# Kernel optimization log

Measured on AMD Instinct MI355X. Metric: run time of the kernel, lower is better.

## Reference

```python
import jax, jax.numpy as jnp
import numpy as np

ALPHA = 4.0          # spikingjelly default surrogate.Sigmoid(alpha=4.0)
V_TH = 1.0           # IFNode default v_threshold
BN_EPS = 1e-5

@jax.custom_vjp
def spike(x):
    # heaviside forward
    return (x >= 0.0).astype(x.dtype)

def _spike_fwd(x):
    return spike(x), x

def _spike_bwd(x, g):
    s = jax.nn.sigmoid(ALPHA * x)
    return (g * ALPHA * s * (1.0 - s),)

spike.defvjp(_spike_fwd, _spike_bwd)

def if_node(x_seq):
    """Multi-step IF neuron: integrate, threshold, hard reset (v_reset=0),
    detach_reset=True. x_seq: [T, ...] -> spikes [T, ...]."""
    def step(v, xt):
        v = v + xt
        s = spike(v - V_TH)
        v = v * (1.0 - jax.lax.stop_gradient(s))  # detached hard reset to 0
        return v, s
    _, s_seq = jax.lax.scan(step, jnp.zeros_like(x_seq[0]), x_seq)
    return s_seq

def bn1d(x, gamma, beta):
    """Training-mode BatchNorm1d over flattened (T*B) batch dim. x: [T,B,F]."""
    m = x.mean(axis=(0, 1))
    v = x.var(axis=(0, 1))  # biased variance, matches torch normalization
    return (x - m) * jax.lax.rsqrt(v + BN_EPS) * gamma + beta

def setup_inputs() -> dict:
    key = jax.random.key(0)
    ks = jax.random.split(key, 12)
    T, B, C, H, W = 8, 64, 2, 128, 128
    F0, D, NC = C * H * W, 2048, 1000
    x = jax.random.uniform(ks[0], (T, B, C, H, W), dtype=jnp.float32)
    def kaiming(k, out_f, in_f):
        # kaiming_normal_ mode='fan_out', relu gain: std = sqrt(2/out_f)
        return jax.random.normal(k, (out_f, in_f), dtype=jnp.float32) * np.sqrt(2.0 / out_f)
    def bias(k, out_f, in_f):
        bound = 1.0 / np.sqrt(in_f)
        return jax.random.uniform(k, (out_f,), dtype=jnp.float32, minval=-bound, maxval=bound)
    inp = {"x": x}
    dims = [(D, F0), (D, D), (D, D)]
    for i, (o, f) in enumerate(dims):
        inp[f"W{i}"] = kaiming(ks[1 + i], o, f)
        inp[f"b{i}"] = bias(ks[4 + i], o, f)
        inp[f"g{i}"] = jnp.ones((o,), jnp.float32)
        inp[f"be{i}"] = jnp.zeros((o,), jnp.float32)
    inp["Wout"] = kaiming(ks[7], NC, D)
    inp["bout"] = bias(ks[8], NC, D)
    return inp

def reference(x, W0, b0, g0, be0, W1, b1, g1, be1, W2, b2, g2, be2, Wout, bout):
    T, B = x.shape[0], x.shape[1]
    h = x.reshape(T, B, -1)           # [T,B,32768]
    h = if_node(h)                    # sn0
    for Wl, bl, gl, bel in ((W0, b0, g0, be0), (W1, b1, g1, be1), (W2, b2, g2, be2)):
        h = jnp.einsum('tbi,oi->tbo', h, Wl) + bl
        h = bn1d(h, gl, bel)
        h = if_node(h)
    out = jnp.einsum('tbi,oi->tbo', h, Wout) + bout  # [T,B,1000]
    return out.mean(axis=0)           # [B,1000]
```

## Files before the change

kernel.cpp:

```cpp
#include <hip/hip_runtime.h>


#define T_STEPS 8
#define BATCH 64
#define F0 32768
#define DIM 2048
#define NROWS 512
#define NC 1000

typedef __attribute__((ext_vector_type(8))) short short8;
typedef __attribute__((ext_vector_type(4))) float f32x4;

__device__ __forceinline__ unsigned short bf16_rne(float f) {
    unsigned int u = __float_as_uint(f);
    u += 0x7FFFu + ((u >> 16) & 1u);
    return (unsigned short)(u >> 16);
}

#define BM 128
#define BN 128
#define BK 64

#define SBAR() do { __builtin_amdgcn_sched_barrier(0); \
                    __builtin_amdgcn_s_barrier();      \
                    __builtin_amdgcn_sched_barrier(0); } while (0)

__device__ __forceinline__ short8 lds_frag(const unsigned short* base, int row, int kb) {
    const int off = row * 128 + (kb ^ ((row & 7) << 4));
    return *(const short8*)((const char*)base + off);
}

__global__ __launch_bounds__(512) void gemm_splitk(
    const unsigned short* __restrict__ A, const float* __restrict__ W,
    float* __restrict__ part, int M, int N, int K, int Kpart, int Wrows)
{
    __shared__ unsigned short As[2][BM * BK];
    __shared__ unsigned short Hs[BN * BK];
    __shared__ unsigned short Ls[BN * BK];

    const int gx = gridDim.x, gy = gridDim.y;
    const int nwg = gx * gy * gridDim.z;
    const int lid = blockIdx.x + gx * (blockIdx.y + gy * blockIdx.z);
    const int cpx = nwg >> 3;
    const int nid = (lid & 7) * cpx + (lid >> 3);
    const int bx  = nid % gx;
    const int by  = (nid / gx) % gy;
    const int kz  = nid / (gx * gy);

    const int tid  = threadIdx.x;
    const int lane = tid & 63;
    const int w    = tid >> 6;
    const int bm   = bx * BM;
    const int bn   = by * BN;
    const int ksteps = Kpart / BK;
    const int wm = (w >> 2) * 64;
    const int wn = (w & 3) * 32;
    const int kbase = kz * Kpart;

    f32x4 acc[4][2] = {};
    float4 wv[4];

    auto issue_loads = [&](int buf, int kt) {
        const int k0 = kbase + kt * BK;
#pragma unroll
        for (int i = 0; i < 4; ++i) {
            const int n  = (tid >> 4) + 32 * i;
            const int c4 = tid & 15;
            const int gn = min(bn + n, Wrows - 1);
            wv[i] = *(const float4*)&W[(size_t)gn * K + k0 + c4 * 4];
        }
#pragma unroll
        for (int c = 0; c < 2; ++c) {
            const int r    = w * 16 + c * 8 + (lane >> 3);
            const int colb = ((lane & 7) * 16) ^ ((r & 7) << 4);
            const char* src = (const char*)A + ((size_t)(bm + r) * K + k0) * 2 + colb;
            unsigned short* dst = &As[buf][(w * 16 + c * 8) * BK];
            __builtin_amdgcn_global_load_lds(
                (const __attribute__((address_space(1))) void*)src,
                (__attribute__((address_space(3))) void*)dst, 16, 0, 0);
        }
    };

    auto convert_write = [&]() {
#pragma unroll
        for (int i = 0; i < 4; ++i) {
            const int n  = (tid >> 4) + 32 * i;
            const int c4 = tid & 15;
            const float vf[4] = {wv[i].x, wv[i].y, wv[i].z, wv[i].w};
            unsigned short h[4], l[4];
#pragma unroll
            for (int e = 0; e < 4; ++e) {
                h[e] = bf16_rne(vf[e]);
                const float hf = __uint_as_float((unsigned int)h[e] << 16);
                l[e] = bf16_rne(vf[e] - hf);
            }
            const int off = n * 128 + ((c4 * 8) ^ ((n & 7) << 4));
            *(ushort4*)((char*)Hs + off) = make_ushort4(h[0], h[1], h[2], h[3]);
            *(ushort4*)((char*)Ls + off) = make_ushort4(l[0], l[1], l[2], l[3]);
        }
    };

    issue_loads(0, 0);
    convert_write();
    asm volatile("s_waitcnt vmcnt(0) lgkmcnt(0)" ::: "memory");
    SBAR();

    int cur = 0;
    for (int kt = 0; kt < ksteps; ++kt) {
        const bool last = (kt + 1 == ksteps);
        if (!last) issue_loads(cur ^ 1, kt + 1);

#pragma unroll
        for (int kk = 0; kk < 2; ++kk) {
            const int kb = (kk * 32 + (lane >> 4) * 8) * 2;
            short8 a[4], bh[2], bl[2];
#pragma unroll
            for (int i = 0; i < 4; ++i)
                a[i] = lds_frag(&As[cur][0], wm + i * 16 + (lane & 15), kb);
#pragma unroll
            for (int i = 0; i < 2; ++i) {
                const int r = wn + i * 16 + (lane & 15);
                bh[i] = lds_frag(Hs, r, kb);
                bl[i] = lds_frag(Ls, r, kb);
            }
#pragma unroll
            for (int mi = 0; mi < 4; ++mi)
#pragma unroll
                for (int ni = 0; ni < 2; ++ni) {
                    acc[mi][ni] = __builtin_amdgcn_mfma_f32_16x16x32_bf16(
                        a[mi], bh[ni], acc[mi][ni], 0, 0, 0);
                    acc[mi][ni] = __builtin_amdgcn_mfma_f32_16x16x32_bf16(
                        a[mi], bl[ni], acc[mi][ni], 0, 0, 0);
                }
        }

        if (!last) {
            SBAR();
            convert_write();
            asm volatile("s_waitcnt vmcnt(0) lgkmcnt(0)" ::: "memory");
            SBAR();
            cur ^= 1;
        }
    }

    const size_t zoff = (size_t)kz * M * N;
#pragma unroll
    for (int mi = 0; mi < 4; ++mi) {
        const int gr0 = bm + wm + mi * 16 + (lane >> 4) * 4;
#pragma unroll
        for (int ni = 0; ni < 2; ++ni) {
            const int gc = bn + wn + ni * 16 + (lane & 15);
            if (gc < N) {
#pragma unroll
                for (int e = 0; e < 4; ++e) {
                    const int gr = gr0 + e;
                    if (gr < M) part[zoff + (size_t)gr * N + gc] = acc[mi][ni][e];
                }
            }
        }
    }
}

__global__ __launch_bounds__(256) void reduce_bias(
    const float* __restrict__ part, const float* __restrict__ bias,
    float* __restrict__ out, int KS, int MN, int N)
{
    const int i4 = blockIdx.x * 256 + threadIdx.x;
    if (i4 * 4 >= MN) return;
    float4 s = make_float4(0.f, 0.f, 0.f, 0.f);
    for (int z = 0; z < KS; ++z) {
        const float4 p = *(const float4*)&part[(size_t)z * MN + i4 * 4];
        s.x += p.x; s.y += p.y; s.z += p.z; s.w += p.w;
    }
    const int col = (i4 * 4) % N;
    const float4 b = *(const float4*)&bias[col];
    s.x += b.x; s.y += b.y; s.z += b.z; s.w += b.w;
    *(float4*)&out[(size_t)i4 * 4] = s;
}

__global__ __launch_bounds__(256) void if0_kernel(
    const float* __restrict__ x, unsigned short* __restrict__ s)
{
    const size_t id4 = ((size_t)blockIdx.x * 256 + threadIdx.x) * 4;
    float v0 = 0.f, v1 = 0.f, v2 = 0.f, v3 = 0.f;
#pragma unroll
    for (int t = 0; t < T_STEPS; ++t) {
        const size_t idx = (size_t)t * (BATCH * (size_t)F0) + id4;
        const float4 xv = *(const float4*)&x[idx];
        ushort4 o;
        v0 += xv.x; if (v0 >= 1.f) { o.x = 0x3F80; v0 = 0.f; } else o.x = 0;
        v1 += xv.y; if (v1 >= 1.f) { o.y = 0x3F80; v1 = 0.f; } else o.y = 0;
        v2 += xv.z; if (v2 >= 1.f) { o.z = 0x3F80; v2 = 0.f; } else o.z = 0;
        v3 += xv.w; if (v3 >= 1.f) { o.w = 0x3F80; v3 = 0.f; } else o.w = 0;
        *(ushort4*)&s[idx] = o;
    }
}

__global__ __launch_bounds__(256) void bn_stats_if(
    const float* __restrict__ z, const float* __restrict__ g,
    const float* __restrict__ be, unsigned short* __restrict__ s)
{
    __shared__ float ssum[4][64], ssq[4][64];
    __shared__ float ssc[64], ssh[64];
    const int l = threadIdx.x & 63;
    const int q = threadIdx.x >> 6;
    const int f = blockIdx.x * 64 + l;
    float sum = 0.f, sq = 0.f;
    for (int r = q; r < NROWS; r += 4) {
        const float v = z[(size_t)r * DIM + f];
        sum += v; sq += v * v;
    }
    ssum[q][l] = sum; ssq[q][l] = sq;
    __syncthreads();
    if (threadIdx.x < 64) {
        float ts = 0.f, tq = 0.f;
#pragma unroll
        for (int i = 0; i < 4; ++i) { ts += ssum[i][l]; tq += ssq[i][l]; }
        const float mean = ts * (1.0f / NROWS);
        const float var  = tq * (1.0f / NROWS) - mean * mean;
        const float inv  = rsqrtf(var + 1e-5f);
        const float sc   = g[f] * inv;
        ssc[l] = sc;
        ssh[l] = be[f] - mean * sc;
    }
    __syncthreads();
    const float sc = ssc[l];
    const float sh = ssh[l];
    for (int b = q; b < BATCH; b += 4) {
        const int id = b * DIM + f;
        float v = 0.f;
#pragma unroll
        for (int t = 0; t < T_STEPS; ++t) {
            const size_t idx = (size_t)t * (BATCH * DIM) + id;
            v += z[idx] * sc + sh;
            if (v >= 1.0f) { s[idx] = 0x3F80; v = 0.f; }
            else           { s[idx] = 0; }
        }
    }
}

__global__ __launch_bounds__(256) void bn_stats_if_mean(
    const float* __restrict__ z, const float* __restrict__ g,
    const float* __restrict__ be, unsigned short* __restrict__ sbar)
{
    __shared__ float ssum[4][64], ssq[4][64];
    __shared__ float ssc[64], ssh[64];
    const int l = threadIdx.x & 63;
    const int q = threadIdx.x >> 6;
    const int f = blockIdx.x * 64 + l;
    float sum = 0.f, sq = 0.f;
    for (int r = q; r < NROWS; r += 4) {
        const float v = z[(size_t)r * DIM + f];
        sum += v; sq += v * v;
    }
    ssum[q][l] = sum; ssq[q][l] = sq;
    __syncthreads();
    if (threadIdx.x < 64) {
        float ts = 0.f, tq = 0.f;
#pragma unroll
        for (int i = 0; i < 4; ++i) { ts += ssum[i][l]; tq += ssq[i][l]; }
        const float mean = ts * (1.0f / NROWS);
        const float var  = tq * (1.0f / NROWS) - mean * mean;
        const float inv  = rsqrtf(var + 1e-5f);
        const float sc   = g[f] * inv;
        ssc[l] = sc;
        ssh[l] = be[f] - mean * sc;
    }
    __syncthreads();
    const float sc = ssc[l];
    const float sh = ssh[l];
    for (int b = q; b < BATCH; b += 4) {
        const int id = b * DIM + f;
        float v = 0.f;
        int cnt = 0;
#pragma unroll
        for (int t = 0; t < T_STEPS; ++t) {
            const size_t idx = (size_t)t * (BATCH * DIM) + id;
            v += z[idx] * sc + sh;
            if (v >= 1.0f) { cnt++; v = 0.f; }
        }
        sbar[id] = bf16_rne((float)cnt * 0.125f);
    }
}

extern "C" void kernel_launch(void* const* d_in, const int* in_sizes, int n_in,
                              void* d_out, int out_size, void* d_ws, size_t ws_size,
                              hipStream_t stream)
{
    const float* x    = (const float*)d_in[0];
    const float* W0   = (const float*)d_in[1];
    const float* b0   = (const float*)d_in[2];
    const float* g0   = (const float*)d_in[3];
    const float* be0  = (const float*)d_in[4];
    const float* W1   = (const float*)d_in[5];
    const float* b1   = (const float*)d_in[6];
    const float* g1   = (const float*)d_in[7];
    const float* be1  = (const float*)d_in[8];
    const float* W2   = (const float*)d_in[9];
    const float* b2   = (const float*)d_in[10];
    const float* g2   = (const float*)d_in[11];
    const float* be2  = (const float*)d_in[12];
    const float* Wout = (const float*)d_in[13];
    const float* bout = (const float*)d_in[14];
    float* out = (float*)d_out;
    (void)in_sizes; (void)n_in; (void)out_size; (void)ws_size;

    char* ws = (char*)d_ws;
    size_t off = 0;
    auto alloc = [&](size_t nbytes) {
        char* p = ws + off;
        off = (off + nbytes + 255) & ~(size_t)255;
        return p;
    };
    unsigned short* s0 = (unsigned short*)alloc((size_t)NROWS * F0 * 2);
    unsigned short* s1 = (unsigned short*)alloc((size_t)NROWS * DIM * 2);
    unsigned short* s2 = (unsigned short*)alloc((size_t)NROWS * DIM * 2);
    unsigned short* sb = (unsigned short*)alloc((size_t)128 * DIM * 2);
    float* z    = (float*)alloc((size_t)NROWS * DIM * 4);
    float* part = (float*)alloc((size_t)16 * NROWS * DIM * 4);

    const int MN = NROWS * DIM;

    if0_kernel<<<(BATCH * (size_t)F0) / 4 / 256, 256, 0, stream>>>(x, s0);

    gemm_splitk<<<dim3(NROWS / BM, DIM / BN, 8), 512, 0, stream>>>(
        s0, W0, part, NROWS, DIM, F0, F0 / 8, DIM);
    reduce_bias<<<MN / 4 / 256, 256, 0, stream>>>(part, b0, z, 8, MN, DIM);
    bn_stats_if<<<DIM / 64, 256, 0, stream>>>(z, g0, be0, s1);

    gemm_splitk<<<dim3(NROWS / BM, DIM / BN, 8), 512, 0, stream>>>(
        s1, W1, part, NROWS, DIM, DIM, DIM / 8, DIM);
    reduce_bias<<<MN / 4 / 256, 256, 0, stream>>>(part, b1, z, 8, MN, DIM);
    bn_stats_if<<<DIM / 64, 256, 0, stream>>>(z, g1, be1, s2);

    gemm_splitk<<<dim3(NROWS / BM, DIM / BN, 8), 512, 0, stream>>>(
        s2, W2, part, NROWS, DIM, DIM, DIM / 8, DIM);
    reduce_bias<<<MN / 4 / 256, 256, 0, stream>>>(part, b2, z, 8, MN, DIM);
    bn_stats_if_mean<<<DIM / 64, 256, 0, stream>>>(z, g2, be2, sb);

    gemm_splitk<<<dim3(1, (NC + BN - 1) / BN, 8), 512, 0, stream>>>(
        sb, Wout, part, BATCH, NC, DIM, DIM / 8, NC);
    reduce_bias<<<(BATCH * NC / 4 + 255) / 256, 256, 0, stream>>>(
        part, bout, out, 8, BATCH * NC, NC);
}
```

Measured before the change: 395.1 us.

## Load W fragments directly into registers, skipping LDS staging, and split K 16 ways

Each lane now loads the fp32 weight values for its own MFMA B fragment straight from global memory. It converts them in registers to hi/lo bf16 pairs, using a packed convert for the low part, so the Hs/Ls LDS buffers, their writes and reads, and one barrier per k-step are gone. The first-layer GEMM also moves from 8-way to 16-way split-K to put more workgroups on the large K=32768 reduction. The cost is that weight global loads lose the coalesced row-per-thread pattern (each lane reads 32-byte pieces from different rows). Register pressure also rises, and the reduction pass has to read twice as many partial buffers for layer 0.

After: 637.8 us. +61.4%, slower.

```diff
diff --git a/kernel.cpp b/kernel.cpp
--- a/kernel.cpp
+++ b/kernel.cpp
@@ -25,18 +25,11 @@
                     __builtin_amdgcn_s_barrier();      \
                     __builtin_amdgcn_sched_barrier(0); } while (0)
 
-__device__ __forceinline__ short8 lds_frag(const unsigned short* base, int row, int kb) {
-    const int off = row * 128 + (kb ^ ((row & 7) << 4));
-    return *(const short8*)((const char*)base + off);
-}
-
 __global__ __launch_bounds__(512) void gemm_splitk(
     const unsigned short* __restrict__ A, const float* __restrict__ W,
     float* __restrict__ part, int M, int N, int K, int Kpart, int Wrows)
 {
     __shared__ unsigned short As[2][BM * BK];
-    __shared__ unsigned short Hs[BN * BK];
-    __shared__ unsigned short Ls[BN * BK];
 
     const int gx = gridDim.x, gy = gridDim.y;
     const int nwg = gx * gy * gridDim.z;
@@ -50,25 +43,39 @@
     const int tid  = threadIdx.x;
     const int lane = tid & 63;
     const int w    = tid >> 6;
+    const int l15  = lane & 15;
+    const int lh   = lane >> 4;
     const int bm   = bx * BM;
     const int bn   = by * BN;
-    const int ksteps = Kpart / BK;
-    const int wm = (w >> 2) * 64;
-    const int wn = (w & 3) * 32;
+    const int ks   = Kpart / BK;
+    const int wm   = (w >> 2) * 64;
+    const int wn   = (w & 3) * 32;
     const int kbase = kz * Kpart;
 
+    size_t wrow[2];
+#pragma unroll
+    for (int ni = 0; ni < 2; ++ni) {
+        const int r = min(bn + wn + ni * 16 + l15, Wrows - 1);
+        wrow[ni] = (size_t)r * K;
+    }
+
     f32x4 acc[4][2] = {};
-    float4 wv[4];
-
-    auto issue_loads = [&](int buf, int kt) {
+    float4 wr[2][2][2];
+    short8 bh[2][2], bl[2][2];
+
+    auto issueW = [&](int kt) {
+        const int k0 = kbase + kt * BK + lh * 8;
+#pragma unroll
+        for (int ni = 0; ni < 2; ++ni)
+#pragma unroll
+            for (int kk = 0; kk < 2; ++kk) {
+                const float* p = W + wrow[ni] + k0 + kk * 32;
+                wr[ni][kk][0] = *(const float4*)p;
+                wr[ni][kk][1] = *(const float4*)(p + 4);
+            }
+    };
+    auto issueA = [&](int buf, int kt) {
         const int k0 = kbase + kt * BK;
-#pragma unroll
-        for (int i = 0; i < 4; ++i) {
-            const int n  = (tid >> 4) + 32 * i;
-            const int c4 = tid & 15;
-            const int gn = min(bn + n, Wrows - 1);
-            wv[i] = *(const float4*)&W[(size_t)gn * K + k0 + c4 * 4];
-        }
 #pragma unroll
         for (int c = 0; c < 2; ++c) {
             const int r    = w * 16 + c * 8 + (lane >> 3);
@@ -80,76 +87,81 @@
                 (__attribute__((address_space(3))) void*)dst, 16, 0, 0);
         }
     };
-
-    auto convert_write = [&]() {
-#pragma unroll
-        for (int i = 0; i < 4; ++i) {
-            const int n  = (tid >> 4) + 32 * i;
-            const int c4 = tid & 15;
-            const float vf[4] = {wv[i].x, wv[i].y, wv[i].z, wv[i].w};
-            unsigned short h[4], l[4];
-#pragma unroll
-            for (int e = 0; e < 4; ++e) {
-                h[e] = bf16_rne(vf[e]);
-                const float hf = __uint_as_float((unsigned int)h[e] << 16);
-                l[e] = bf16_rne(vf[e] - hf);
+    auto convertW = [&]() {
+#pragma unroll
+        for (int ni = 0; ni < 2; ++ni)
+#pragma unroll
+            for (int kk = 0; kk < 2; ++kk) {
+                const float vf[8] = {wr[ni][kk][0].x, wr[ni][kk][0].y,
+                                     wr[ni][kk][0].z, wr[ni][kk][0].w,
+                                     wr[ni][kk][1].x, wr[ni][kk][1].y,
+                                     wr[ni][kk][1].z, wr[ni][kk][1].w};
+                unsigned hw[4], lw[4];
+#pragma unroll
+                for (int p = 0; p < 4; ++p) {
+                    const unsigned ua = __float_as_uint(vf[2 * p]);
+                    const unsigned ub = __float_as_uint(vf[2 * p + 1]);
+                    const unsigned ra = (ua + 0x7FFFu + ((ua >> 16) & 1u)) & 0xFFFF0000u;
+                    const unsigned rb = (ub + 0x7FFFu + ((ub >> 16) & 1u)) & 0xFFFF0000u;
+                    hw[p] = (ra >> 16) | rb;
+                    const float la = vf[2 * p]     - __uint_as_float(ra);
+                    const float lb = vf[2 * p + 1] - __uint_as_float(rb);
+                    unsigned lo;
+                    asm("v_cvt_pk_bf16_f32 %0, %1, %2" : "=v"(lo) : "v"(la), "v"(lb));
+                    lw[p] = lo;
+                }
+                uint4 hv = make_uint4(hw[0], hw[1], hw[2], hw[3]);
+                uint4 lv = make_uint4(lw[0], lw[1], lw[2], lw[3]);
+                bh[ni][kk] = *(short8*)&hv;
+                bl[ni][kk] = *(short8*)&lv;
             }
-            const int off = n * 128 + ((c4 * 8) ^ ((n & 7) << 4));
-            *(ushort4*)((char*)Hs + off) = make_ushort4(h[0], h[1], h[2], h[3]);
-            *(ushort4*)((char*)Ls + off) = make_ushort4(l[0], l[1], l[2], l[3]);
-        }
-    };
-
-    issue_loads(0, 0);
-    convert_write();
+    };
+    auto mfmaStep = [&](int cb) {
+#pragma unroll
+        for (int kk = 0; kk < 2; ++kk) {
+            const int kb = (kk * 32 + lh * 8) * 2;
+#pragma unroll
+            for (int mi = 0; mi < 4; ++mi) {
+                const int r = wm + mi * 16 + l15;
+                const short8 a = *(const short8*)(
+                    (const char*)&As[cb][0] + r * 128 + (kb ^ ((r & 7) << 4)));
+#pragma unroll
+                for (int ni = 0; ni < 2; ++ni) {
+                    acc[mi][ni] = __builtin_amdgcn_mfma_f32_16x16x32_bf16(
+                        a, bh[ni][kk], acc[mi][ni], 0, 0, 0);
+                    acc[mi][ni] = __builtin_amdgcn_mfma_f32_16x16x32_bf16(
+                        a, bl[ni][kk], acc[mi][ni], 0, 0, 0);
+                }
+            }
+        }
+    };
+
+    issueW(0);
+    issueA(0, 0);
+    convertW();
     asm volatile("s_waitcnt vmcnt(0) lgkmcnt(0)" ::: "memory");
     SBAR();
 
-    int cur = 0;
-    for (int kt = 0; kt < ksteps; ++kt) {
-        const bool last = (kt + 1 == ksteps);
-        if (!last) issue_loads(cur ^ 1, kt + 1);
-
-#pragma unroll
-        for (int kk = 0; kk < 2; ++kk) {
-            const int kb = (kk * 32 + (lane >> 4) * 8) * 2;
-            short8 a[4], bh[2], bl[2];
-#pragma unroll
-            for (int i = 0; i < 4; ++i)
-                a[i] = lds_frag(&As[cur][0], wm + i * 16 + (lane & 15), kb);
-#pragma unroll
-            for (int i = 0; i < 2; ++i) {
-                const int r = wn + i * 16 + (lane & 15);
-                bh[i] = lds_frag(Hs, r, kb);
-                bl[i] = lds_frag(Ls, r, kb);
-            }
-#pragma unroll
-            for (int mi = 0; mi < 4; ++mi)
-#pragma unroll
-                for (int ni = 0; ni < 2; ++ni) {
-                    acc[mi][ni] = __builtin_amdgcn_mfma_f32_16x16x32_bf16(
-                        a[mi], bh[ni], acc[mi][ni], 0, 0, 0);
-                    acc[mi][ni] = __builtin_amdgcn_mfma_f32_16x16x32_bf16(
-                        a[mi], bl[ni], acc[mi][ni], 0, 0, 0);
-                }
-        }
-
+    int cb = 0;
+    for (int t = 0; t < ks; ++t) {
+        const bool last = (t + 1 == ks);
+        if (!last) { issueW(t + 1); issueA(cb ^ 1, t + 1); }
+        mfmaStep(cb);
         if (!last) {
-            SBAR();
-            convert_write();
+            convertW();
             asm volatile("s_waitcnt vmcnt(0) lgkmcnt(0)" ::: "memory");
             SBAR();
-            cur ^= 1;
+            cb ^= 1;
         }
     }
 
     const size_t zoff = (size_t)kz * M * N;
 #pragma unroll
     for (int mi = 0; mi < 4; ++mi) {
-        const int gr0 = bm + wm + mi * 16 + (lane >> 4) * 4;
+        const int gr0 = bm + wm + mi * 16 + lh * 4;
 #pragma unroll
         for (int ni = 0; ni < 2; ++ni) {
-            const int gc = bn + wn + ni * 16 + (lane & 15);
+            const int gc = bn + wn + ni * 16 + l15;
             if (gc < N) {
 #pragma unroll
                 for (int e = 0; e < 4; ++e) {
@@ -323,9 +335,9 @@
 
     if0_kernel<<<(BATCH * (size_t)F0) / 4 / 256, 256, 0, stream>>>(x, s0);
 
-    gemm_splitk<<<dim3(NROWS / BM, DIM / BN, 8), 512, 0, stream>>>(
-        s0, W0, part, NROWS, DIM, F0, F0 / 8, DIM);
-    reduce_bias<<<MN / 4 / 256, 256, 0, stream>>>(part, b0, z, 8, MN, DIM);
+    gemm_splitk<<<dim3(NROWS / BM, DIM / BN, 16), 512, 0, stream>>>(
+        s0, W0, part, NROWS, DIM, F0, F0 / 16, DIM);
+    reduce_bias<<<MN / 4 / 256, 256, 0, stream>>>(part, b0, z, 16, MN, DIM);
     bn_stats_if<<<DIM / 64, 256, 0, stream>>>(z, g0, be0, s1);
 
     gemm_splitk<<<dim3(NROWS / BM, DIM / BN, 8), 512, 0, stream>>>(
```
